# Optimization experiments

Measured on AMD Instinct MI355X. Metric: run time of the kernel, lower is better.

## Reference

```python
import jax, jax.numpy as jnp
import numpy as np

B, N, NIN, NHID, D = 8, 2048, 256, 256, 64  # head = 1 (required by squeeze())


def setup_inputs() -> dict:
    key = jax.random.key(0)
    ks = jax.random.split(key, 12)
    xn = lambda k, shape, s=1.0: jax.random.normal(k, shape, jnp.float32) * s
    xav = lambda fi, fo: (2.0 / (fi + fo)) ** 0.5  # xavier_normal std
    return {
        "inputs": xn(ks[0], (B, N, NIN)),
        "fc1_w": xn(ks[1], (NHID, NIN), xav(NIN, NHID)),
        "fc1_b": jnp.full((NHID,), 0.1, jnp.float32),
        "fc2_w": xn(ks[2], (NHID, NHID), xav(NHID, NHID)),
        "fc2_b": jnp.full((NHID,), 0.1, jnp.float32),
        "bn_g": 1.0 + 0.1 * xn(ks[3], (NHID,)),
        "bn_b": 0.1 * xn(ks[4], (NHID,)),
        "bn_mean": 0.1 * xn(ks[5], (NHID,)),
        "bn_var": jax.random.uniform(ks[6], (NHID,), jnp.float32, 0.5, 1.5),
        "wq_w": xn(ks[7], (D, NHID), xav(NHID, D)),
        "wq_b": jnp.full((D,), 0.1, jnp.float32),
        "wk_w": xn(ks[8], (D, NHID), xav(NHID, D)),
        "wk_b": jnp.full((D,), 0.1, jnp.float32),
        "mlp2_w": xn(ks[9], (1, 2 * D), xav(2 * D, 1)),
        "mlp2_b": jnp.full((1,), 0.1, jnp.float32),
    }


def reference(inputs, fc1_w, fc1_b, fc2_w, fc2_b, bn_g, bn_b, bn_mean, bn_var,
              wq_w, wq_b, wk_w, wk_b, mlp2_w, mlp2_b):
    # MLP: Linear -> ELU -> (dropout off, eval) -> Linear -> ELU -> BatchNorm1d (eval, running stats)
    x = jax.nn.elu(jnp.einsum('bni,hi->bnh', inputs, fc1_w) + fc1_b)
    x = jax.nn.elu(jnp.einsum('bnh,oh->bno', x, fc2_w) + fc2_b)
    X = (x - bn_mean) * jax.lax.rsqrt(bn_var + 1e-5) * bn_g + bn_b  # [B,N,NHID]
    # Q/K projections (head=1 -> shapes [B,N,D])
    Xq = jnp.einsum('bnh,dh->bnd', X, wq_w) + wq_b
    Xk = jnp.einsum('bnh,dh->bnd', X, wk_w) + wk_b
    # Original: cat([NK, NQ], -1) over all (i,j) pairs then Linear(2D -> 1).
    # Algebraically identical decomposition: probs[b,i,j] = Xk[b,j].wk_half + Xq[b,i].wq_half + bias
    wk_half, wq_half = mlp2_w[0, :D], mlp2_w[0, D:]
    sk = Xk @ wk_half  # [B,N]  (varies with j, the K/column index)
    sq = Xq @ wq_half  # [B,N]  (varies with i, the Q/row index)
    probs = sq[:, :, None] + sk[:, None, :] + mlp2_b[0]  # [B,N,N]
    return probs
```

## Files before the change

### kernel.cpp

```cpp
#include <hip/hip_runtime.h>
#include <hip/hip_bf16.h>
#include <math.h>

typedef __bf16 bf16x8 __attribute__((ext_vector_type(8)));
typedef float  f32x4  __attribute__((ext_vector_type(4)));

#define WS_STG1  0
#define WS_STG2  65536
#define WS_UQ    131072
#define WS_UK    131328
#define WS_CONST 131584
#define WS_SQ    131600
#define WS_SK    148000

__device__ __forceinline__ float elu1(float x) { return x > 0.f ? x : expm1f(x); }

__global__ void prep_all(const float* __restrict__ w1, const float* __restrict__ w2,
                         const float* __restrict__ bn_g, const float* __restrict__ bn_b,
                         const float* __restrict__ bn_mean, const float* __restrict__ bn_var,
                         const float* __restrict__ wq_w, const float* __restrict__ wq_b,
                         const float* __restrict__ wk_w, const float* __restrict__ wk_b,
                         const float* __restrict__ mlp2_w, const float* __restrict__ mlp2_b,
                         float* __restrict__ ws) {
    if (blockIdx.x == 0) {
        __shared__ float redq[256], redk[256];
        const int h = threadIdx.x;
        float s  = bn_g[h] * rsqrtf(bn_var[h] + 1e-5f);
        float tt = bn_b[h] - bn_mean[h] * s;
        float vq = 0.f, vk = 0.f;
        #pragma unroll
        for (int d = 0; d < 64; ++d) {
            vq += wq_w[d * 256 + h] * mlp2_w[64 + d];
            vk += wk_w[d * 256 + h] * mlp2_w[d];
        }
        ws[WS_UQ + h] = s * vq;
        ws[WS_UK + h] = s * vk;
        redq[h] = tt * vq;
        redk[h] = tt * vk;
        __syncthreads();
        for (int st = 128; st > 0; st >>= 1) {
            if (h < st) { redq[h] += redq[h + st]; redk[h] += redk[h + st]; }
            __syncthreads();
        }
        if (h == 0) {
            float cq = 0.f, ck = 0.f;
            for (int d = 0; d < 64; ++d) {
                cq += wq_b[d] * mlp2_w[64 + d];
                ck += wk_b[d] * mlp2_w[d];
            }
            ws[WS_CONST + 0] = redq[0] + cq;
            ws[WS_CONST + 1] = redk[0] + ck;
            ws[WS_CONST + 2] = mlp2_b[0];
        }
        return;
    }
    const int bid = blockIdx.x - 1;
    const int m   = bid >> 3;
    const int kt  = bid & 7;
    const float* src = m ? w2 : w1;
    __bf16* stgh = (__bf16*)(ws + (m ? WS_STG2 : WS_STG1));
    __bf16* stgl = stgh + 65536;
    const int tid = threadIdx.x;
    #pragma unroll
    for (int it = 0; it < 4; ++it) {
        int idx = it * 256 + tid;
        int nt = idx >> 6, l = idx & 63;
        int lr = l & 15, lk = l >> 4;
        const float* sp = src + (nt * 16 + lr) * 256 + kt * 32 + lk * 8;
        bf16x8 hi, lo;
        #pragma unroll
        for (int j = 0; j < 8; ++j) {
            float v = sp[j];
            __bf16 hb = (__bf16)v;
            hi[j] = hb;
            lo[j] = (__bf16)(v - (float)hb);
        }
        int off = (kt * 16 + nt) * 512 + l * 8;
        *(bf16x8*)(stgh + off) = hi;
        *(bf16x8*)(stgl + off) = lo;
    }
}

__global__ __launch_bounds__(256, 2) void main_mfma(const float* __restrict__ inp,
                                                    const float* __restrict__ b1,
                                                    const float* __restrict__ b2,
                                                    float* __restrict__ ws) {
    __shared__ float X1s[8192];
    __shared__ float redq[128], redk[128];

    const int tid = threadIdx.x;
    const int l   = tid & 63;
    const int w   = tid >> 6;
    const int lr  = l & 15;
    const int lk  = l >> 4;
    const int rows0 = blockIdx.x * 32;
    const int n0  = w * 64;

    const __bf16* s1 = (const __bf16*)(ws + WS_STG1);
    const __bf16* s2 = (const __bf16*)(ws + WS_STG2);

    f32x4 acc[2][4];

    #pragma unroll
    for (int p = 0; p < 2; ++p)
        #pragma unroll
        for (int nt = 0; nt < 4; ++nt) acc[p][nt] = (f32x4)0.f;

    #pragma unroll 2
    for (int kt = 0; kt < 8; ++kt) {
        bf16x8 bh[4], bl[4];
        #pragma unroll
        for (int nt = 0; nt < 4; ++nt) {
            const __bf16* bp = s1 + ((kt * 16 + w * 4 + nt) << 9) + l * 8;
            bh[nt] = *(const bf16x8*)bp;
            bl[nt] = *(const bf16x8*)(bp + 65536);
        }
        bf16x8 ah[2], al[2];
        #pragma unroll
        for (int p = 0; p < 2; ++p) {
            const float4* ap = (const float4*)(inp + (size_t)(rows0 + p * 16 + lr) * 256 + kt * 32 + lk * 8);
            float4 f0 = ap[0], f1 = ap[1];
            float fv[8] = {f0.x,f0.y,f0.z,f0.w,f1.x,f1.y,f1.z,f1.w};
            #pragma unroll
            for (int j = 0; j < 8; ++j) { __bf16 hv=(__bf16)fv[j]; ah[p][j]=hv; al[p][j]=(__bf16)(fv[j]-(float)hv); }
        }
        #pragma unroll
        for (int p = 0; p < 2; ++p)
            #pragma unroll
            for (int nt = 0; nt < 4; ++nt) {
                acc[p][nt] = __builtin_amdgcn_mfma_f32_16x16x32_bf16(ah[p], bh[nt], acc[p][nt], 0, 0, 0);
                acc[p][nt] = __builtin_amdgcn_mfma_f32_16x16x32_bf16(al[p], bh[nt], acc[p][nt], 0, 0, 0);
                acc[p][nt] = __builtin_amdgcn_mfma_f32_16x16x32_bf16(ah[p], bl[nt], acc[p][nt], 0, 0, 0);
            }
    }
    #pragma unroll
    for (int p = 0; p < 2; ++p)
        #pragma unroll
        for (int nt = 0; nt < 4; ++nt) {
            int col = n0 + nt * 16 + lr;
            float bb = b1[col];
            #pragma unroll
            for (int r = 0; r < 4; ++r) {
                int rr = p * 16 + lk * 4 + r;
                float v = elu1(acc[p][nt][r] + bb);
                int ob = (rr * 1024 + col * 4) ^ ((rr & 7) << 4);
                *(float*)((char*)X1s + ob) = v;
            }
        }
    __syncthreads();

    #pragma unroll
    for (int p = 0; p < 2; ++p)
        #pragma unroll
        for (int nt = 0; nt < 4; ++nt) acc[p][nt] = (f32x4)0.f;

    #pragma unroll 2
    for (int kt = 0; kt < 8; ++kt) {
        bf16x8 bh[4], bl[4];
        #pragma unroll
        for (int nt = 0; nt < 4; ++nt) {
            const __bf16* bp = s2 + ((kt * 16 + w * 4 + nt) << 9) + l * 8;
            bh[nt] = *(const bf16x8*)bp;
            bl[nt] = *(const bf16x8*)(bp + 65536);
        }
        bf16x8 ah[2], al[2];
        #pragma unroll
        for (int p = 0; p < 2; ++p) {
            int rr = p * 16 + lr;
            int ob1 = (rr * 1024 + kt * 128 + lk * 32) ^ ((rr & 7) << 4);
            float4 x0  = *(const float4*)((const char*)X1s + ob1);
            float4 x1v = *(const float4*)((const char*)X1s + (ob1 ^ 16));
            float fv[8] = {x0.x,x0.y,x0.z,x0.w,x1v.x,x1v.y,x1v.z,x1v.w};
            #pragma unroll
            for (int j = 0; j < 8; ++j) { __bf16 hv=(__bf16)fv[j]; ah[p][j]=hv; al[p][j]=(__bf16)(fv[j]-(float)hv); }
        }
        #pragma unroll
        for (int p = 0; p < 2; ++p)
            #pragma unroll
            for (int nt = 0; nt < 4; ++nt) {
                acc[p][nt] = __builtin_amdgcn_mfma_f32_16x16x32_bf16(ah[p], bh[nt], acc[p][nt], 0, 0, 0);
                acc[p][nt] = __builtin_amdgcn_mfma_f32_16x16x32_bf16(al[p], bh[nt], acc[p][nt], 0, 0, 0);
                acc[p][nt] = __builtin_amdgcn_mfma_f32_16x16x32_bf16(ah[p], bl[nt], acc[p][nt], 0, 0, 0);
            }
    }

    float sqp[2][4] = {{0.f,0.f,0.f,0.f},{0.f,0.f,0.f,0.f}};
    float skp[2][4] = {{0.f,0.f,0.f,0.f},{0.f,0.f,0.f,0.f}};
    const float* uq = ws + WS_UQ;
    const float* uk = ws + WS_UK;
    #pragma unroll
    for (int p = 0; p < 2; ++p)
        #pragma unroll
        for (int nt = 0; nt < 4; ++nt) {
            int col = n0 + nt * 16 + lr;
            float bb = b2[col], qc = uq[col], kc = uk[col];
            #pragma unroll
            for (int r = 0; r < 4; ++r) {
                float v = elu1(acc[p][nt][r] + bb);
                sqp[p][r] += v * qc;
                skp[p][r] += v * kc;
            }
        }
    #pragma unroll
    for (int mm = 8; mm >= 1; mm >>= 1) {
        #pragma unroll
        for (int p = 0; p < 2; ++p)
            #pragma unroll
            for (int r = 0; r < 4; ++r) {
                sqp[p][r] += __shfl_xor(sqp[p][r], mm);
                skp[p][r] += __shfl_xor(skp[p][r], mm);
            }
    }
    if (lr == 0) {
        #pragma unroll
        for (int p = 0; p < 2; ++p)
            #pragma unroll
            for (int r = 0; r < 4; ++r) {
                int rl = p * 16 + lk * 4 + r;
                redq[w * 32 + rl] = sqp[p][r];
                redk[w * 32 + rl] = skp[p][r];
            }
    }
    __syncthreads();
    if (tid < 32) {
        float dq = ws[WS_CONST + 0];
        ws[WS_SQ + rows0 + tid] = redq[tid] + redq[32 + tid] + redq[64 + tid] + redq[96 + tid] + dq;
    } else if (tid < 64) {
        int rl = tid - 32;
        float dk = ws[WS_CONST + 1];
        ws[WS_SK + rows0 + rl] = redk[rl] + redk[32 + rl] + redk[64 + rl] + redk[96 + rl] + dk;
    }
}

__global__ __launch_bounds__(256) void broadcast_out(const float* __restrict__ ws,
                                                     float* __restrict__ out) {
    __shared__ float skL[2048];
    const int bi = blockIdx.x;
    const int b = bi >> 8;
    const int chunk = bi & 255;
    const int tid = threadIdx.x;

    float4* skL4 = (float4*)skL;
    const float4* skb4 = (const float4*)(ws + WS_SK + b * 2048);
    #pragma unroll
    for (int it = 0; it < 2; ++it) skL4[it * 256 + tid] = skb4[it * 256 + tid];
    __syncthreads();

    const float mb = ws[WS_CONST + 2];
    const int i0 = chunk * 8;
    #pragma unroll
    for (int i = 0; i < 8; ++i) {
        float sval = ws[WS_SQ + b * 2048 + i0 + i] + mb;
        float4* orow = (float4*)(out + ((size_t)(b * 2048 + i0 + i)) * 2048);
        #pragma unroll
        for (int hh = 0; hh < 2; ++hh) {
            int j4 = hh * 256 + tid;
            float4 v = skL4[j4];
            orow[j4] = make_float4(sval + v.x, sval + v.y, sval + v.z, sval + v.w);
        }
    }
}

extern "C" void kernel_launch(void* const* d_in, const int* in_sizes, int n_in,
                              void* d_out, int out_size, void* d_ws, size_t ws_size,
                              hipStream_t stream) {
    const float* inputs  = (const float*)d_in[0];
    const float* fc1_w   = (const float*)d_in[1];
    const float* fc1_b   = (const float*)d_in[2];
    const float* fc2_w   = (const float*)d_in[3];
    const float* fc2_b   = (const float*)d_in[4];
    const float* bn_g    = (const float*)d_in[5];
    const float* bn_b    = (const float*)d_in[6];
    const float* bn_mean = (const float*)d_in[7];
    const float* bn_var  = (const float*)d_in[8];
    const float* wq_w    = (const float*)d_in[9];
    const float* wq_b    = (const float*)d_in[10];
    const float* wk_w    = (const float*)d_in[11];
    const float* wk_b    = (const float*)d_in[12];
    const float* mlp2_w  = (const float*)d_in[13];
    const float* mlp2_b  = (const float*)d_in[14];
    float* ws  = (float*)d_ws;
    float* out = (float*)d_out;

    hipLaunchKernelGGL(prep_all, dim3(17), dim3(256), 0, stream,
                       fc1_w, fc2_w, bn_g, bn_b, bn_mean, bn_var,
                       wq_w, wq_b, wk_w, wk_b, mlp2_w, mlp2_b, ws);
    hipLaunchKernelGGL(main_mfma, dim3(512), dim3(256), 0, stream,
                       inputs, fc1_b, fc2_b, ws);
    hipLaunchKernelGGL(broadcast_out, dim3(2048), dim3(256), 0, stream, ws, out);
}
```

Measured before the change: 58.82 us.

## Drop weight low-part MFMAs, pack hi/lo bf16 in LDS, 8 waves, nontemporal stores

The weights are now kept only as single bf16, so the weight-low staging buffer and one of the three split-precision MFMAs per tile are removed. Layer-1 activations are stored in LDS as packed hi/lo bf16 pairs and unpacked with perm instructions instead of being re-split from fp32. The main kernel moves to 512 threads with 8 waves, each covering 32 columns, and the reduction loops over 8 partials. ELU uses a fast __expf and the broadcast kernel writes with nontemporal stores. Dropping the weight low part reduces accuracy and risks exceeding the tolerance.

```diff
diff --git a/kernel.cpp b/kernel.cpp
--- a/kernel.cpp
+++ b/kernel.cpp
@@ -4,16 +4,21 @@
 
 typedef __bf16 bf16x8 __attribute__((ext_vector_type(8)));
 typedef float  f32x4  __attribute__((ext_vector_type(4)));
+typedef unsigned int u32;
+typedef u32 u32x4 __attribute__((ext_vector_type(4)));
+typedef unsigned short u16;
 
 #define WS_STG1  0
-#define WS_STG2  65536
-#define WS_UQ    131072
-#define WS_UK    131328
-#define WS_CONST 131584
-#define WS_SQ    131600
-#define WS_SK    148000
-
-__device__ __forceinline__ float elu1(float x) { return x > 0.f ? x : expm1f(x); }
+#define WS_STG2  32768
+#define WS_UQ    65536
+#define WS_UK    65792
+#define WS_CONST 66048
+#define WS_SQ    66064
+#define WS_SK    82448
+
+__device__ __forceinline__ float elu1(float x) {
+    return x > 0.f ? x : (__expf(x) - 1.f);
+}
 
 __global__ void prep_all(const float* __restrict__ w1, const float* __restrict__ w2,
                          const float* __restrict__ bn_g, const float* __restrict__ bn_b,
@@ -58,8 +63,7 @@
     const int m   = bid >> 3;
     const int kt  = bid & 7;
     const float* src = m ? w2 : w1;
-    __bf16* stgh = (__bf16*)(ws + (m ? WS_STG2 : WS_STG1));
-    __bf16* stgl = stgh + 65536;
+    __bf16* stg = (__bf16*)(ws + (m ? WS_STG2 : WS_STG1));
     const int tid = threadIdx.x;
     #pragma unroll
     for (int it = 0; it < 4; ++it) {
@@ -67,26 +71,19 @@
         int nt = idx >> 6, l = idx & 63;
         int lr = l & 15, lk = l >> 4;
         const float* sp = src + (nt * 16 + lr) * 256 + kt * 32 + lk * 8;
-        bf16x8 hi, lo;
-        #pragma unroll
-        for (int j = 0; j < 8; ++j) {
-            float v = sp[j];
-            __bf16 hb = (__bf16)v;
-            hi[j] = hb;
-            lo[j] = (__bf16)(v - (float)hb);
-        }
-        int off = (kt * 16 + nt) * 512 + l * 8;
-        *(bf16x8*)(stgh + off) = hi;
-        *(bf16x8*)(stgl + off) = lo;
-    }
-}
-
-__global__ __launch_bounds__(256, 2) void main_mfma(const float* __restrict__ inp,
+        bf16x8 hi;
+        #pragma unroll
+        for (int j = 0; j < 8; ++j) hi[j] = (__bf16)sp[j];
+        *(bf16x8*)(stg + (kt * 16 + nt) * 512 + l * 8) = hi;
+    }
+}
+
+__global__ __launch_bounds__(512, 4) void main_mfma(const float* __restrict__ inp,
                                                     const float* __restrict__ b1,
                                                     const float* __restrict__ b2,
                                                     float* __restrict__ ws) {
-    __shared__ float X1s[8192];
-    __shared__ float redq[128], redk[128];
+    __shared__ u32 X1p[8192];
+    __shared__ float redq[256], redk[256];
 
     const int tid = threadIdx.x;
     const int l   = tid & 63;
@@ -94,27 +91,24 @@
     const int lr  = l & 15;
     const int lk  = l >> 4;
     const int rows0 = blockIdx.x * 32;
-    const int n0  = w * 64;
+    const int n0  = w * 32;
 
     const __bf16* s1 = (const __bf16*)(ws + WS_STG1);
     const __bf16* s2 = (const __bf16*)(ws + WS_STG2);
 
-    f32x4 acc[2][4];
+    f32x4 acc[2][2];
 
     #pragma unroll
     for (int p = 0; p < 2; ++p)
         #pragma unroll
-        for (int nt = 0; nt < 4; ++nt) acc[p][nt] = (f32x4)0.f;
+        for (int nt = 0; nt < 2; ++nt) acc[p][nt] = (f32x4)0.f;
 
     #pragma unroll 2
     for (int kt = 0; kt < 8; ++kt) {
-        bf16x8 bh[4], bl[4];
-        #pragma unroll
-        for (int nt = 0; nt < 4; ++nt) {
-            const __bf16* bp = s1 + ((kt * 16 + w * 4 + nt) << 9) + l * 8;
-            bh[nt] = *(const bf16x8*)bp;
-            bl[nt] = *(const bf16x8*)(bp + 65536);
-        }
+        bf16x8 bh[2];
+        #pragma unroll
+        for (int nt = 0; nt < 2; ++nt)
+            bh[nt] = *(const bf16x8*)(s1 + ((kt * 16 + w * 2 + nt) << 9) + l * 8);
         bf16x8 ah[2], al[2];
         #pragma unroll
         for (int p = 0; p < 2; ++p) {
@@ -122,29 +116,35 @@
             float4 f0 = ap[0], f1 = ap[1];
             float fv[8] = {f0.x,f0.y,f0.z,f0.w,f1.x,f1.y,f1.z,f1.w};
             #pragma unroll
-            for (int j = 0; j < 8; ++j) { __bf16 hv=(__bf16)fv[j]; ah[p][j]=hv; al[p][j]=(__bf16)(fv[j]-(float)hv); }
+            for (int j = 0; j < 8; ++j) {
+                __bf16 hv = (__bf16)fv[j];
+                ah[p][j] = hv;
+                al[p][j] = (__bf16)(fv[j] - (float)hv);
+            }
         }
         #pragma unroll
         for (int p = 0; p < 2; ++p)
             #pragma unroll
-            for (int nt = 0; nt < 4; ++nt) {
+            for (int nt = 0; nt < 2; ++nt) {
                 acc[p][nt] = __builtin_amdgcn_mfma_f32_16x16x32_bf16(ah[p], bh[nt], acc[p][nt], 0, 0, 0);
                 acc[p][nt] = __builtin_amdgcn_mfma_f32_16x16x32_bf16(al[p], bh[nt], acc[p][nt], 0, 0, 0);
-                acc[p][nt] = __builtin_amdgcn_mfma_f32_16x16x32_bf16(ah[p], bl[nt], acc[p][nt], 0, 0, 0);
             }
     }
     #pragma unroll
     for (int p = 0; p < 2; ++p)
         #pragma unroll
-        for (int nt = 0; nt < 4; ++nt) {
+        for (int nt = 0; nt < 2; ++nt) {
             int col = n0 + nt * 16 + lr;
             float bb = b1[col];
             #pragma unroll
             for (int r = 0; r < 4; ++r) {
-                int rr = p * 16 + lk * 4 + r;
+                int row = p * 16 + lk * 4 + r;
                 float v = elu1(acc[p][nt][r] + bb);
-                int ob = (rr * 1024 + col * 4) ^ ((rr & 7) << 4);
-                *(float*)((char*)X1s + ob) = v;
+                __bf16 hv = (__bf16)v;
+                __bf16 lv = (__bf16)(v - (float)hv);
+                u32 pk = ((u32)__builtin_bit_cast(u16, hv) << 16) | __builtin_bit_cast(u16, lv);
+                int ob = row * 1024 + ((col * 4) ^ ((row & 15) << 4));
+                *(u32*)((char*)X1p + ob) = pk;
             }
         }
     __syncthreads();
@@ -152,35 +152,42 @@
     #pragma unroll
     for (int p = 0; p < 2; ++p)
         #pragma unroll
-        for (int nt = 0; nt < 4; ++nt) acc[p][nt] = (f32x4)0.f;
+        for (int nt = 0; nt < 2; ++nt) acc[p][nt] = (f32x4)0.f;
 
     #pragma unroll 2
     for (int kt = 0; kt < 8; ++kt) {
-        bf16x8 bh[4], bl[4];
-        #pragma unroll
-        for (int nt = 0; nt < 4; ++nt) {
-            const __bf16* bp = s2 + ((kt * 16 + w * 4 + nt) << 9) + l * 8;
-            bh[nt] = *(const bf16x8*)bp;
-            bl[nt] = *(const bf16x8*)(bp + 65536);
-        }
+        bf16x8 bh[2];
+        #pragma unroll
+        for (int nt = 0; nt < 2; ++nt)
+            bh[nt] = *(const bf16x8*)(s2 + ((kt * 16 + w * 2 + nt) << 9) + l * 8);
         bf16x8 ah[2], al[2];
         #pragma unroll
         for (int p = 0; p < 2; ++p) {
-            int rr = p * 16 + lr;
-            int ob1 = (rr * 1024 + kt * 128 + lk * 32) ^ ((rr & 7) << 4);
-            float4 x0  = *(const float4*)((const char*)X1s + ob1);
-            float4 x1v = *(const float4*)((const char*)X1s + (ob1 ^ 16));
-            float fv[8] = {x0.x,x0.y,x0.z,x0.w,x1v.x,x1v.y,x1v.z,x1v.w};
-            #pragma unroll
-            for (int j = 0; j < 8; ++j) { __bf16 hv=(__bf16)fv[j]; ah[p][j]=hv; al[p][j]=(__bf16)(fv[j]-(float)hv); }
+            int row = p * 16 + lr;
+            int base = row * 1024;
+            int cb = kt * 128 + lk * 32;
+            int sw = (row & 15) << 4;
+            u32x4 q0 = *(const u32x4*)((const char*)X1p + base + (cb ^ sw));
+            u32x4 q1 = *(const u32x4*)((const char*)X1p + base + ((cb + 16) ^ sw));
+            u32 hw0 = __builtin_amdgcn_perm(q0.y, q0.x, 0x07060302u);
+            u32 hw1 = __builtin_amdgcn_perm(q0.w, q0.z, 0x07060302u);
+            u32 hw2 = __builtin_amdgcn_perm(q1.y, q1.x, 0x07060302u);
+            u32 hw3 = __builtin_amdgcn_perm(q1.w, q1.z, 0x07060302u);
+            u32 lw0 = __builtin_amdgcn_perm(q0.y, q0.x, 0x05040100u);
+            u32 lw1 = __builtin_amdgcn_perm(q0.w, q0.z, 0x05040100u);
+            u32 lw2 = __builtin_amdgcn_perm(q1.y, q1.x, 0x05040100u);
+            u32 lw3 = __builtin_amdgcn_perm(q1.w, q1.z, 0x05040100u);
+            u32x4 hh = {hw0, hw1, hw2, hw3};
+            u32x4 ll = {lw0, lw1, lw2, lw3};
+            ah[p] = __builtin_bit_cast(bf16x8, hh);
+            al[p] = __builtin_bit_cast(bf16x8, ll);
         }
         #pragma unroll
         for (int p = 0; p < 2; ++p)
             #pragma unroll
-            for (int nt = 0; nt < 4; ++nt) {
+            for (int nt = 0; nt < 2; ++nt) {
                 acc[p][nt] = __builtin_amdgcn_mfma_f32_16x16x32_bf16(ah[p], bh[nt], acc[p][nt], 0, 0, 0);
                 acc[p][nt] = __builtin_amdgcn_mfma_f32_16x16x32_bf16(al[p], bh[nt], acc[p][nt], 0, 0, 0);
-                acc[p][nt] = __builtin_amdgcn_mfma_f32_16x16x32_bf16(ah[p], bl[nt], acc[p][nt], 0, 0, 0);
             }
     }
 
@@ -191,7 +198,7 @@
     #pragma unroll
     for (int p = 0; p < 2; ++p)
         #pragma unroll
-        for (int nt = 0; nt < 4; ++nt) {
+        for (int nt = 0; nt < 2; ++nt) {
             int col = n0 + nt * 16 + lr;
             float bb = b2[col], qc = uq[col], kc = uk[col];
             #pragma unroll
@@ -224,11 +231,17 @@
     __syncthreads();
     if (tid < 32) {
         float dq = ws[WS_CONST + 0];
-        ws[WS_SQ + rows0 + tid] = redq[tid] + redq[32 + tid] + redq[64 + tid] + redq[96 + tid] + dq;
+        float s = dq;
+        #pragma unroll
+        for (int ww = 0; ww < 8; ++ww) s += redq[ww * 32 + tid];
+        ws[WS_SQ + rows0 + tid] = s;
     } else if (tid < 64) {
         int rl = tid - 32;
         float dk = ws[WS_CONST + 1];
-        ws[WS_SK + rows0 + rl] = redk[rl] + redk[32 + rl] + redk[64 + rl] + redk[96 + rl] + dk;
+        float s = dk;
+        #pragma unroll
+        for (int ww = 0; ww < 8; ++ww) s += redk[ww * 32 + rl];
+        ws[WS_SK + rows0 + rl] = s;
     }
 }
 
@@ -251,12 +264,13 @@
     #pragma unroll
     for (int i = 0; i < 8; ++i) {
         float sval = ws[WS_SQ + b * 2048 + i0 + i] + mb;
-        float4* orow = (float4*)(out + ((size_t)(b * 2048 + i0 + i)) * 2048);
+        f32x4* orow = (f32x4*)(out + ((size_t)(b * 2048 + i0 + i)) * 2048);
         #pragma unroll
         for (int hh = 0; hh < 2; ++hh) {
             int j4 = hh * 256 + tid;
             float4 v = skL4[j4];
-            orow[j4] = make_float4(sval + v.x, sval + v.y, sval + v.z, sval + v.w);
+            f32x4 o = {sval + v.x, sval + v.y, sval + v.z, sval + v.w};
+            __builtin_nontemporal_store(o, &orow[j4]);
         }
     }
 }
@@ -285,7 +299,7 @@
     hipLaunchKernelGGL(prep_all, dim3(17), dim3(256), 0, stream,
                        fc1_w, fc2_w, bn_g, bn_b, bn_mean, bn_var,
                        wq_w, wq_b, wk_w, wk_b, mlp2_w, mlp2_b, ws);
-    hipLaunchKernelGGL(main_mfma, dim3(512), dim3(256), 0, stream,
+    hipLaunchKernelGGL(main_mfma, dim3(512), dim3(512), 0, stream,
                        inputs, fc1_b, fc2_b, ws);
     hipLaunchKernelGGL(broadcast_out, dim3(2048), dim3(256), 0, stream, ws, out);
 }
```

Result: slower. 60.66 us (+3.1%).
